# Kernel optimization log

Hardware: AMD Instinct MI355X
Metric: run time of the kernel (lower is better)

Reference implementation:

```python
import jax, jax.numpy as jnp
import numpy as np

T, B, I, H, FC, C = 256, 256, 1024, 256, 128, 8  # seq, batch, input, hidden, fc1, classes


def setup_inputs() -> dict:
    key = jax.random.key(0)
    ks = jax.random.split(key, 9)
    s_ih = 1.0 / np.sqrt(H)
    return {
        "x": jax.random.normal(ks[0], (T, B, I), dtype=jnp.float32),
        "W_ih": jax.random.uniform(ks[1], (4 * H, I), jnp.float32, -s_ih, s_ih),
        "W_hh": jax.random.uniform(ks[2], (4 * H, H), jnp.float32, -s_ih, s_ih),
        "b_ih": jax.random.uniform(ks[3], (4 * H,), jnp.float32, -s_ih, s_ih),
        "b_hh": jax.random.uniform(ks[4], (4 * H,), jnp.float32, -s_ih, s_ih),
        "W1": jax.random.uniform(ks[5], (FC, H), jnp.float32, -s_ih, s_ih),
        "b1": jax.random.uniform(ks[6], (FC,), jnp.float32, -s_ih, s_ih),
        "W2": jax.random.uniform(ks[7], (C, FC), jnp.float32, -1.0 / np.sqrt(FC), 1.0 / np.sqrt(FC)),
        "b2": jax.random.uniform(ks[8], (C,), jnp.float32, -1.0 / np.sqrt(FC), 1.0 / np.sqrt(FC)),
    }


def _lstm(x, W_ih, W_hh, b_ih, b_hh):
    # x: [T, B, I]; PyTorch gate order: i, f, g, o
    xg = jnp.einsum("tbi,gi->tbg", x, W_ih) + b_ih + b_hh  # precompute input projections [T,B,4H]

    def step(carry, xg_t):
        h, c = carry
        z = xg_t + h @ W_hh.T  # [B, 4H]
        i, f, g, o = jnp.split(z, 4, axis=-1)
        i = jax.nn.sigmoid(i)
        f = jax.nn.sigmoid(f)
        g = jnp.tanh(g)
        o = jax.nn.sigmoid(o)
        c = f * c + i * g
        h = o * jnp.tanh(c)
        return (h, c), h

    h0 = jnp.zeros((x.shape[1], W_hh.shape[1]), x.dtype)
    (hn, cn), out = jax.lax.scan(step, (h0, h0), xg)
    return out  # [T, B, H]


def reference(x, W_ih, W_hh, b_ih, b_hh, W1, b1, W2, b2):
    out = _lstm(x, W_ih, W_hh, b_ih, b_hh)      # [T, B, H]
    out = jax.nn.relu(out)
    out = jax.nn.relu(out @ W1.T + b1)           # [T, B, 128]
    out = out @ W2.T + b2                        # [T, B, num_classes]
    return out
```

## Files before the change

### kernel.cpp

```cpp
#include <hip/hip_runtime.h>
#include <type_traits>


typedef float    f4    __attribute__((ext_vector_type(4)));
typedef float    f32x4 __attribute__((ext_vector_type(4)));
typedef _Float16 h8    __attribute__((ext_vector_type(8)));
typedef _Float16 h4    __attribute__((ext_vector_type(4)));

__device__ __forceinline__ float ldf(const float* p)    { return *p; }
__device__ __forceinline__ float ldf(const _Float16* p) { return (float)*p; }

__device__ __forceinline__ float fast_sigmoid(float x) {
    return 1.f / (1.f + __expf(-x));
}
__device__ __forceinline__ float fast_tanh(float x) {
    const float e = __expf(-2.f * fabsf(x));
    const float t = (1.f - e) / (1.f + e);
    return copysignf(t, x);
}

__global__ __launch_bounds__(256) void k_bias(const float* __restrict__ b_ih,
                                              const float* __restrict__ b_hh,
                                              float* __restrict__ bias) {
    const int i = blockIdx.x * 256 + threadIdx.x;
    if (i < 1024) bias[i] = b_ih[i] + b_hh[i];
}

__global__ __launch_bounds__(256) void k_pack(const float* __restrict__ W_hh,
                                              _Float16* __restrict__ Wp) {
    const int idx = blockIdx.x * 256 + threadIdx.x;
    const int fi = idx >> 6;
    const int l  = idx & 63;
    const int g  = (fi >> 3) * 16 + (l & 15);
    const int k  = (fi & 7) * 32 + ((l >> 4) << 3);
    const float* src = &W_hh[(size_t)g * 256 + k];
    h8 v;
    #pragma unroll
    for (int c = 0; c < 8; ++c) v[c] = (_Float16)src[c];
    *(h8*)&Wp[(size_t)idx * 8] = v;
}

__global__ __launch_bounds__(256) void k_xg_mfma(
    const float* __restrict__ x, const float* __restrict__ W_ih,
    const float* __restrict__ bias, _Float16* __restrict__ xg2)
{
    __shared__ _Float16 As[2][128][40];
    __shared__ _Float16 Bs[2][128][40];
    const int tid = threadIdx.x;
    const int l   = tid & 63;
    const int w   = tid >> 6;
    const int bid = blockIdx.y * 8 + blockIdx.x;
    const int swz = (bid & 7) * 512 + (bid >> 3);
    const int m0  = (swz >> 3) * 128;
    const int n0  = (swz & 7) * 128;
    const int wr  = (w >> 1) * 64;
    const int wc  = (w & 1) * 64;
    const int srow = tid >> 2;
    const int skof = (tid & 3) * 8;
    const int lr = l & 15;
    const int lg = l >> 4;

    f32x4 acc[4][4] = {};
    f4 ldA[2][2], ldB[2][2];

    auto XG_LOAD = [&](int kt) {
        const int k0 = kt * 32;
        #pragma unroll
        for (int s = 0; s < 2; ++s) {
            const float* xa = &x[(size_t)(m0 + srow + s * 64) * 1024 + k0 + skof];
            const float* wb = &W_ih[(size_t)(n0 + srow + s * 64) * 1024 + k0 + skof];
            ldA[s][0] = *(const f4*)xa; ldA[s][1] = *(const f4*)(xa + 4);
            ldB[s][0] = *(const f4*)wb; ldB[s][1] = *(const f4*)(wb + 4);
        }
    };
    auto XG_WRITE = [&](int buf) {
        #pragma unroll
        for (int s = 0; s < 2; ++s) {
            h8 va, vb;
            #pragma unroll
            for (int c = 0; c < 8; ++c) {
                va[c] = (_Float16)ldA[s][c >> 2][c & 3];
                vb[c] = (_Float16)ldB[s][c >> 2][c & 3];
            }
            *(h8*)&As[buf][srow + s * 64][skof] = va;
            *(h8*)&Bs[buf][srow + s * 64][skof] = vb;
        }
    };

    XG_LOAD(0);
    XG_WRITE(0);
    __syncthreads();
    for (int kt = 0; kt < 32; ++kt) {
        const int cur = kt & 1;
        if (kt + 1 < 32) XG_LOAD(kt + 1);
        h8 af[4], bf[4];
        #pragma unroll
        for (int mf = 0; mf < 4; ++mf) af[mf] = *(const h8*)&As[cur][wr + mf * 16 + lr][lg * 8];
        #pragma unroll
        for (int nf = 0; nf < 4; ++nf) bf[nf] = *(const h8*)&Bs[cur][wc + nf * 16 + lr][lg * 8];
        #pragma unroll
        for (int mf = 0; mf < 4; ++mf)
            #pragma unroll
            for (int nf = 0; nf < 4; ++nf)
                acc[mf][nf] = __builtin_amdgcn_mfma_f32_16x16x32_f16(af[mf], bf[nf], acc[mf][nf], 0, 0, 0);
        if (kt + 1 < 32) XG_WRITE((kt + 1) & 1);
        __syncthreads();
    }
    #pragma unroll
    for (int nf = 0; nf < 4; ++nf) {
        const int col  = n0 + wc + nf * 16 + lr;
        const float bv = bias[col];
        const int gate = col >> 8;
        const int w8   = (col >> 5) & 7;
        const int jt   = (col >> 4) & 1;
        #pragma unroll
        for (int mf = 0; mf < 4; ++mf) {
            const int rowb = m0 + wr + mf * 16 + lg * 4;
            const int tt = rowb >> 8;
            const int gb = (rowb >> 4) & 15;
            h4 pk;
            #pragma unroll
            for (int r = 0; r < 4; ++r) pk[r] = (_Float16)(acc[mf][nf][r] + bv);
            *(h4*)&xg2[((((size_t)tt * 16 + gb) * 8 + w8) * 64 + l) * 32 + gate * 8 + jt * 4] = pk;
        }
    }
}

__global__ __launch_bounds__(512, 2) void k_lstm_8w(
    const _Float16* __restrict__ xg2, const _Float16* __restrict__ Wp,
    _Float16* __restrict__ h_all)
{
    __shared__ _Float16 wlds[8 * 17 * 512];
    __shared__ _Float16 h_sh[2][16][264];
    const int tid = threadIdx.x;
    const int w  = tid >> 6;
    const int l  = tid & 63;
    const int lr = l & 15;
    const int lg = l >> 4;
    const int g  = blockIdx.x;
    const int b0 = g * 16;

    auto fgid = [&](int ti, int kb) {
        return (((ti >> 1) * 16 + w * 2 + (ti & 1)) * 8 + kb);
    };
    auto ldfrag = [&](int ti, int kb) {
        return *(const h8*)&Wp[((size_t)fgid(ti, kb) * 64 + l) * 8];
    };

    h8 wvg[24];
    #pragma unroll
    for (int kb = 0; kb < 3; ++kb)
        #pragma unroll
        for (int ti = 0; ti < 8; ++ti)
            wvg[kb * 8 + ti] = ldfrag(ti, kb);

    #pragma unroll
    for (int ti = 0; ti < 8; ++ti)
        *(h8*)&wlds[((w * 17 + ti) * 64 + l) * 8] = ldfrag(ti, 3);
    #pragma unroll
    for (int ti = 0; ti < 8; ++ti)
        *(h8*)&wlds[((w * 17 + 8 + ti) * 64 + l) * 8] = ldfrag(ti, 4);
    *(h8*)&wlds[((w * 17 + 16) * 64 + l) * 8] = ldfrag(0, 5);

    {
        _Float16* p = &h_sh[0][0][0];
        for (int i = tid; i < 2 * 16 * 264; i += 512) p[i] = (_Float16)0.f;
    }
    __syncthreads();

    float c[8];
    #pragma unroll
    for (int i = 0; i < 8; ++i) c[i] = 0.f;

    for (int t = 0; t < 256; ++t) {
        const int cur = t & 1;
        const int nxt = cur ^ 1;

        const size_t E = ((((size_t)t * 16 + g) * 8 + w) * 64 + l) * 32;
        h8 xq[4];
        #pragma unroll
        for (int q = 0; q < 4; ++q) xq[q] = *(const h8*)&xg2[E + q * 8];

        unsigned soff = 0;
        asm volatile("" : "+v"(soff));
        h8 sv[23];
        #pragma unroll
        for (int ti = 1; ti < 8; ++ti)
            sv[ti - 1] = *(const h8*)&Wp[((size_t)fgid(ti, 5) * 64 + l) * 8 + soff];
        #pragma unroll
        for (int ti = 0; ti < 8; ++ti)
            sv[7 + ti] = *(const h8*)&Wp[((size_t)fgid(ti, 6) * 64 + l) * 8 + soff];
        #pragma unroll
        for (int ti = 0; ti < 8; ++ti)
            sv[15 + ti] = *(const h8*)&Wp[((size_t)fgid(ti, 7) * 64 + l) * 8 + soff];

        f32x4 acc[8];
        #pragma unroll
        for (int ti = 0; ti < 8; ++ti) {
            #pragma unroll
            for (int r = 0; r < 4; ++r)
                acc[ti][r] = (float)xq[ti >> 1][(ti & 1) * 4 + r];
        }

        #pragma unroll
        for (int kb = 0; kb < 8; ++kb) {
            const h8 av = *(const h8*)&h_sh[cur][lr][kb * 32 + lg * 8];
            #pragma unroll
            for (int ti = 0; ti < 8; ++ti) {
                h8 b;
                if (kb < 3)                  b = wvg[kb * 8 + ti];
                else if (kb == 3)            b = *(const h8*)&wlds[((w * 17 + ti) * 64 + l) * 8];
                else if (kb == 4)            b = *(const h8*)&wlds[((w * 17 + 8 + ti) * 64 + l) * 8];
                else if (kb == 5 && ti == 0) b = *(const h8*)&wlds[((w * 17 + 16) * 64 + l) * 8];
                else if (kb == 5)            b = sv[ti - 1];
                else if (kb == 6)            b = sv[7 + ti];
                else                         b = sv[15 + ti];
                acc[ti] = __builtin_amdgcn_mfma_f32_16x16x32_f16(av, b, acc[ti], 0, 0, 0);
            }
        }

        #pragma unroll
        for (int jt = 0; jt < 2; ++jt) {
            #pragma unroll
            for (int r = 0; r < 4; ++r) {
                const float ig = fast_sigmoid(acc[0 * 2 + jt][r]);
                const float fg = fast_sigmoid(acc[1 * 2 + jt][r]);
                const float gg = fast_tanh(acc[2 * 2 + jt][r]);
                const float og = fast_sigmoid(acc[3 * 2 + jt][r]);
                const int ci = jt * 4 + r;
                c[ci] = fg * c[ci] + ig * gg;
                const float hv = og * fast_tanh(c[ci]);
                const _Float16 h16 = (_Float16)hv;
                h_sh[nxt][lg * 4 + r][w * 32 + jt * 16 + lr] = h16;
                h_all[((size_t)t * 256 + b0 + lg * 4 + r) * 256 + w * 32 + jt * 16 + lr] = h16;
            }
        }
        __syncthreads();
    }
}

template <typename HT>
__global__ __launch_bounds__(256) void k_fc(
    const HT* __restrict__ h_all, const float* __restrict__ W1,
    const float* __restrict__ b1, const float* __restrict__ W2,
    const float* __restrict__ b2, float* __restrict__ out)
{
    __shared__ __align__(16) float smem[12288];
    float* hsT = smem;
    float* w1T = smem + 4096;
    const int tid = threadIdx.x;
    const int m0 = blockIdx.x * 64;
    const int tx = tid & 15;
    const int ty = tid >> 4;
    const int r0 = ty * 4;
    const int fA = tx * 4;
    const int fB = 64 + tx * 4;
    float acc[4][8] = {};
    for (int kc = 0; kc < 4; ++kc) {
        const int k0 = kc * 64;
        __syncthreads();
        #pragma unroll
        for (int i = 0; i < 4; ++i) {
            const int fid = tid + i * 256;
            const int rr = fid >> 4;
            const int qq = fid & 15;
            const HT* p = &h_all[(size_t)(m0 + rr) * 256 + k0 + qq * 4];
            f4 v;
            if constexpr (std::is_same<HT, float>::value) {
                v = *(const f4*)p;
            } else {
                v[0] = ldf(p); v[1] = ldf(p + 1); v[2] = ldf(p + 2); v[3] = ldf(p + 3);
            }
            #pragma unroll
            for (int cc = 0; cc < 4; ++cc)
                hsT[(qq * 4 + cc) * 64 + rr] = fmaxf(v[cc], 0.f);
        }
        #pragma unroll
        for (int i = 0; i < 8; ++i) {
            const int fid = tid + i * 256;
            const int ff = fid >> 4;
            const int qq = fid & 15;
            const f4 v = *(const f4*)&W1[(size_t)ff * 256 + k0 + qq * 4];
            #pragma unroll
            for (int cc = 0; cc < 4; ++cc)
                w1T[(qq * 4 + cc) * 128 + ff] = v[cc];
        }
        __syncthreads();
        #pragma unroll 4
        for (int kk = 0; kk < 64; ++kk) {
            const f4 aa = *(const f4*)&hsT[kk * 64 + r0];
            const f4 ba = *(const f4*)&w1T[kk * 128 + fA];
            const f4 bb = *(const f4*)&w1T[kk * 128 + fB];
            #pragma unroll
            for (int i = 0; i < 4; ++i) {
                #pragma unroll
                for (int j = 0; j < 4; ++j) {
                    acc[i][j]     = fmaf(aa[i], ba[j], acc[i][j]);
                    acc[i][j + 4] = fmaf(aa[i], bb[j], acc[i][j + 4]);
                }
            }
        }
    }
    __syncthreads();
    float* fc1s = smem;
    #pragma unroll
    for (int j = 0; j < 4; ++j) {
        const float bbA = b1[fA + j];
        const float bbB = b1[fB + j];
        #pragma unroll
        for (int i = 0; i < 4; ++i) {
            fc1s[(r0 + i) * 132 + fA + j] = fmaxf(acc[i][j] + bbA, 0.f);
            fc1s[(r0 + i) * 132 + fB + j] = fmaxf(acc[i][j + 4] + bbB, 0.f);
        }
    }
    __syncthreads();
    const int r  = tid >> 2;
    const int c0 = (tid & 3) * 2;
    float o0 = b2[c0], o1 = b2[c0 + 1];
    #pragma unroll
    for (int fq = 0; fq < 32; ++fq) {
        const f4 p  = *(const f4*)&fc1s[r * 132 + fq * 4];
        const f4 wa = *(const f4*)&W2[(size_t)c0 * 128 + fq * 4];
        const f4 wb = *(const f4*)&W2[(size_t)(c0 + 1) * 128 + fq * 4];
        o0 += p[0] * wa[0] + p[1] * wa[1] + p[2] * wa[2] + p[3] * wa[3];
        o1 += p[0] * wb[0] + p[1] * wb[1] + p[2] * wb[2] + p[3] * wb[3];
    }
    out[(size_t)(m0 + r) * 8 + c0]     = o0;
    out[(size_t)(m0 + r) * 8 + c0 + 1] = o1;
}

extern "C" void kernel_launch(void* const* d_in, const int* in_sizes, int n_in,
                              void* d_out, int out_size, void* d_ws, size_t ws_size,
                              hipStream_t stream)
{
    const float* x    = (const float*)d_in[0];
    const float* W_ih = (const float*)d_in[1];
    const float* W_hh = (const float*)d_in[2];
    const float* b_ih = (const float*)d_in[3];
    const float* b_hh = (const float*)d_in[4];
    const float* W1   = (const float*)d_in[5];
    const float* b1   = (const float*)d_in[6];
    const float* W2   = (const float*)d_in[7];
    const float* b2   = (const float*)d_in[8];
    float* out = (float*)d_out;
    char* ws = (char*)d_ws;

    _Float16* xg2   = (_Float16*)ws;
    _Float16* h_all = (_Float16*)(ws + 134217728);
    _Float16* Wp    = (_Float16*)(ws + 167772160);
    float*    bias  = (float*)   (ws + 168296448);

    k_bias<<<4, 256, 0, stream>>>(b_ih, b_hh, bias);
    k_pack<<<128, 256, 0, stream>>>(W_hh, Wp);
    k_xg_mfma<<<dim3(8, 512), 256, 0, stream>>>(x, W_ih, bias, xg2);
    k_lstm_8w<<<16, 512, 0, stream>>>(xg2, Wp, h_all);
    k_fc<_Float16><<<1024, 256, 0, stream>>>(h_all, W1, b1, W2, b2, out);
}
```

Measured before the change: 1.897 ms.

## Rewrite FC head with fp16 MFMA and pre-packed W1 fragments

Replaces the scalar FP32 FMA tiled FC1 kernel with an MFMA 16x16x32 f16 kernel. W1 is pre-packed into fragment order by a new pack kernel, and the packed buffer reuses the W_hh pack workspace after the LSTM finishes. The kernel applies ReLU to h in fp16 registers, processes 128 rows per block, and vectorises the FC2 output stores. This removes the FMA-bound FC1 cost and the per-element fp16 loads, but adds an extra launch and quantises W1 to fp16.

```diff
diff --git a/kernel.cpp b/kernel.cpp
--- a/kernel.cpp
+++ b/kernel.cpp
@@ -6,9 +6,6 @@
 typedef float    f32x4 __attribute__((ext_vector_type(4)));
 typedef _Float16 h8    __attribute__((ext_vector_type(8)));
 typedef _Float16 h4    __attribute__((ext_vector_type(4)));
-
-__device__ __forceinline__ float ldf(const float* p)    { return *p; }
-__device__ __forceinline__ float ldf(const _Float16* p) { return (float)*p; }
 
 __device__ __forceinline__ float fast_sigmoid(float x) {
     return 1.f / (1.f + __expf(-x));
@@ -38,6 +35,20 @@
     #pragma unroll
     for (int c = 0; c < 8; ++c) v[c] = (_Float16)src[c];
     *(h8*)&Wp[(size_t)idx * 8] = v;
+}
+
+__global__ __launch_bounds__(256) void k_pack1(const float* __restrict__ W1,
+                                               _Float16* __restrict__ Wp1) {
+    const int idx = blockIdx.x * 256 + threadIdx.x;
+    const int fi = idx >> 6;
+    const int l  = idx & 63;
+    const int row = (fi >> 3) * 16 + (l & 15);
+    const int k   = (fi & 7) * 32 + ((l >> 4) << 3);
+    const float* src = &W1[(size_t)row * 256 + k];
+    h8 v;
+    #pragma unroll
+    for (int c = 0; c < 8; ++c) v[c] = (_Float16)src[c];
+    *(h8*)&Wp1[(size_t)idx * 8] = v;
 }
 
 __global__ __launch_bounds__(256) void k_xg_mfma(
@@ -239,94 +250,73 @@
     }
 }
 
-template <typename HT>
-__global__ __launch_bounds__(256) void k_fc(
-    const HT* __restrict__ h_all, const float* __restrict__ W1,
+__global__ __launch_bounds__(256) void k_fc_mfma(
+    const _Float16* __restrict__ h_all, const _Float16* __restrict__ Wp1,
     const float* __restrict__ b1, const float* __restrict__ W2,
     const float* __restrict__ b2, float* __restrict__ out)
 {
-    __shared__ __align__(16) float smem[12288];
-    float* hsT = smem;
-    float* w1T = smem + 4096;
+    __shared__ _Float16 w1f[64 * 512];
+    __shared__ float    fc1s[128 * 132];
     const int tid = threadIdx.x;
-    const int m0 = blockIdx.x * 64;
-    const int tx = tid & 15;
-    const int ty = tid >> 4;
-    const int r0 = ty * 4;
-    const int fA = tx * 4;
-    const int fB = 64 + tx * 4;
-    float acc[4][8] = {};
-    for (int kc = 0; kc < 4; ++kc) {
-        const int k0 = kc * 64;
-        __syncthreads();
-        #pragma unroll
-        for (int i = 0; i < 4; ++i) {
-            const int fid = tid + i * 256;
-            const int rr = fid >> 4;
-            const int qq = fid & 15;
-            const HT* p = &h_all[(size_t)(m0 + rr) * 256 + k0 + qq * 4];
-            f4 v;
-            if constexpr (std::is_same<HT, float>::value) {
-                v = *(const f4*)p;
-            } else {
-                v[0] = ldf(p); v[1] = ldf(p + 1); v[2] = ldf(p + 2); v[3] = ldf(p + 3);
-            }
-            #pragma unroll
-            for (int cc = 0; cc < 4; ++cc)
-                hsT[(qq * 4 + cc) * 64 + rr] = fmaxf(v[cc], 0.f);
-        }
-        #pragma unroll
-        for (int i = 0; i < 8; ++i) {
-            const int fid = tid + i * 256;
-            const int ff = fid >> 4;
-            const int qq = fid & 15;
-            const f4 v = *(const f4*)&W1[(size_t)ff * 256 + k0 + qq * 4];
-            #pragma unroll
-            for (int cc = 0; cc < 4; ++cc)
-                w1T[(qq * 4 + cc) * 128 + ff] = v[cc];
-        }
-        __syncthreads();
-        #pragma unroll 4
-        for (int kk = 0; kk < 64; ++kk) {
-            const f4 aa = *(const f4*)&hsT[kk * 64 + r0];
-            const f4 ba = *(const f4*)&w1T[kk * 128 + fA];
-            const f4 bb = *(const f4*)&w1T[kk * 128 + fB];
-            #pragma unroll
-            for (int i = 0; i < 4; ++i) {
-                #pragma unroll
-                for (int j = 0; j < 4; ++j) {
-                    acc[i][j]     = fmaf(aa[i], ba[j], acc[i][j]);
-                    acc[i][j + 4] = fmaf(aa[i], bb[j], acc[i][j + 4]);
-                }
-            }
-        }
+    const int w  = tid >> 6;
+    const int l  = tid & 63;
+    const int lr = l & 15;
+    const int lg = l >> 4;
+    const int m0 = blockIdx.x * 128;
+
+    #pragma unroll
+    for (int i = 0; i < 16; ++i) {
+        const int idx = tid + i * 256;
+        *(h8*)&w1f[idx * 8] = *(const h8*)&Wp1[(size_t)idx * 8];
     }
     __syncthreads();
-    float* fc1s = smem;
-    #pragma unroll
-    for (int j = 0; j < 4; ++j) {
-        const float bbA = b1[fA + j];
-        const float bbB = b1[fB + j];
-        #pragma unroll
-        for (int i = 0; i < 4; ++i) {
-            fc1s[(r0 + i) * 132 + fA + j] = fmaxf(acc[i][j] + bbA, 0.f);
-            fc1s[(r0 + i) * 132 + fB + j] = fmaxf(acc[i][j + 4] + bbB, 0.f);
+
+    f32x4 acc[2][8] = {};
+    #pragma unroll
+    for (int kb = 0; kb < 8; ++kb) {
+        h8 a[2];
+        #pragma unroll
+        for (int mt = 0; mt < 2; ++mt) {
+            h8 v = *(const h8*)&h_all[(size_t)(m0 + w * 32 + mt * 16 + lr) * 256 + kb * 32 + lg * 8];
+            #pragma unroll
+            for (int cc = 0; cc < 8; ++cc)
+                v[cc] = v[cc] > (_Float16)0.f ? v[cc] : (_Float16)0.f;
+            a[mt] = v;
+        }
+        #pragma unroll
+        for (int nt = 0; nt < 8; ++nt) {
+            const h8 b = *(const h8*)&w1f[((nt * 8 + kb) * 64 + l) * 8];
+            acc[0][nt] = __builtin_amdgcn_mfma_f32_16x16x32_f16(a[0], b, acc[0][nt], 0, 0, 0);
+            acc[1][nt] = __builtin_amdgcn_mfma_f32_16x16x32_f16(a[1], b, acc[1][nt], 0, 0, 0);
+        }
+    }
+    #pragma unroll
+    for (int nt = 0; nt < 8; ++nt) {
+        const int col = nt * 16 + lr;
+        const float bv = b1[col];
+        #pragma unroll
+        for (int mt = 0; mt < 2; ++mt) {
+            const int row = w * 32 + mt * 16 + lg * 4;
+            #pragma unroll
+            for (int r = 0; r < 4; ++r)
+                fc1s[(row + r) * 132 + col] = fmaxf(acc[mt][nt][r] + bv, 0.f);
         }
     }
     __syncthreads();
-    const int r  = tid >> 2;
-    const int c0 = (tid & 3) * 2;
-    float o0 = b2[c0], o1 = b2[c0 + 1];
-    #pragma unroll
+
+    const int r  = tid >> 1;
+    const int c0 = (tid & 1) * 4;
+    float o[4] = {b2[c0], b2[c0 + 1], b2[c0 + 2], b2[c0 + 3]};
+    #pragma unroll 8
     for (int fq = 0; fq < 32; ++fq) {
-        const f4 p  = *(const f4*)&fc1s[r * 132 + fq * 4];
-        const f4 wa = *(const f4*)&W2[(size_t)c0 * 128 + fq * 4];
-        const f4 wb = *(const f4*)&W2[(size_t)(c0 + 1) * 128 + fq * 4];
-        o0 += p[0] * wa[0] + p[1] * wa[1] + p[2] * wa[2] + p[3] * wa[3];
-        o1 += p[0] * wb[0] + p[1] * wb[1] + p[2] * wb[2] + p[3] * wb[3];
-    }
-    out[(size_t)(m0 + r) * 8 + c0]     = o0;
-    out[(size_t)(m0 + r) * 8 + c0 + 1] = o1;
+        const f4 p = *(const f4*)&fc1s[r * 132 + fq * 4];
+        #pragma unroll
+        for (int cc = 0; cc < 4; ++cc) {
+            const f4 wv = *(const f4*)&W2[(size_t)(c0 + cc) * 128 + fq * 4];
+            o[cc] += p[0] * wv[0] + p[1] * wv[1] + p[2] * wv[2] + p[3] * wv[3];
+        }
+    }
+    *(f4*)&out[(size_t)(m0 + r) * 8 + c0] = *(f4*)o;
 }
 
 extern "C" void kernel_launch(void* const* d_in, const int* in_sizes, int n_in,
@@ -349,10 +339,12 @@
     _Float16* h_all = (_Float16*)(ws + 134217728);
     _Float16* Wp    = (_Float16*)(ws + 167772160);
     float*    bias  = (float*)   (ws + 168296448);
+    _Float16* Wp1   = Wp;
 
     k_bias<<<4, 256, 0, stream>>>(b_ih, b_hh, bias);
     k_pack<<<128, 256, 0, stream>>>(W_hh, Wp);
     k_xg_mfma<<<dim3(8, 512), 256, 0, stream>>>(x, W_ih, bias, xg2);
     k_lstm_8w<<<16, 512, 0, stream>>>(xg2, Wp, h_all);
-    k_fc<_Float16><<<1024, 256, 0, stream>>>(h_all, W1, b1, W2, b2, out);
-}
+    k_pack1<<<16, 256, 0, stream>>>(W1, Wp1);
+    k_fc_mfma<<<512, 256, 0, stream>>>(h_all, Wp1, b1, W2, b2, out);
+}
```

Measured after the change: 1.822 ms. -4.0%, faster.
